# Kernel tuning notes

Hardware: AMD Instinct MI355X
Metric: run time of the kernel (lower is better)

Reference implementation:

```python
import jax, jax.numpy as jnp
import numpy as np

BN_EPS = 1e-5


def setup_inputs() -> dict:
    key = jax.random.key(0)
    ks = jax.random.split(key, 8)
    B, C, N = 2, 64, 8192
    s = 1.0 / np.sqrt(C)
    return {
        "feature": jax.random.normal(ks[0], (B, C, N, 1), dtype=jnp.float32),
        "wa": jax.random.normal(ks[1], (C, C), dtype=jnp.float32) * s,
        "ba": jnp.zeros((C,), jnp.float32),
        "wb": jax.random.normal(ks[2], (C, C), dtype=jnp.float32) * s,
        "bb": jnp.zeros((C,), jnp.float32),
        "wm": jax.random.normal(ks[3], (C, C), dtype=jnp.float32) * s,
        "bm": jnp.zeros((C,), jnp.float32),
        "bn_gamma": jnp.ones((C,), jnp.float32),
        "bn_beta": jnp.zeros((C,), jnp.float32),
        "bn_mean": jax.random.normal(ks[4], (C,), dtype=jnp.float32) * 0.1,
        "bn_var": jnp.ones((C,), jnp.float32) + jax.random.uniform(ks[5], (C,), dtype=jnp.float32),
        "alpha": jnp.array(0.5, jnp.float32),
    }


def _pam(feature, wa, ba, wb, bb, wm, bm, g, bt, mean, var, alpha):
    # feature: [B, C, N, 1]
    x = feature[..., 0]  # [B, C, N]
    a = jnp.einsum('oc,bcn->bon', wa, x) + ba[None, :, None]  # fc_a, 1x1 conv
    b = jnp.einsum('oc,bcn->bon', wb, x) + bb[None, :, None]  # fc_b
    # att = a^T b : [B, N, N], softmax over last dim (dim=2)
    att = jax.nn.softmax(jnp.einsum('bcn,bcm->bnm', a, b), axis=2)
    # mlp branch: 1x1 conv + inference BatchNorm
    m = jnp.einsum('oc,bcn->bon', wm, x) + bm[None, :, None]
    m = (m - mean[None, :, None]) * jax.lax.rsqrt(var + BN_EPS)[None, :, None]
    m = m * g[None, :, None] + bt[None, :, None]
    # (att @ m^T)^T : out[b,c,n] = sum_m att[b,n,m] * m[b,c,m]
    out = jnp.einsum('bnm,bcm->bcn', att, m)
    return feature + alpha * out[..., None]


def reference(feature, wa, ba, wb, bb, wm, bm, bn_gamma, bn_beta, bn_mean, bn_var, alpha):
    # GFA calls self.pam twice (fam is unused in its forward): f1 + f2 == 2 * pam(feature)
    p = _pam(feature, wa, ba, wb, bb, wm, bm, bn_gamma, bn_beta, bn_mean, bn_var, alpha)
    return p + p
```

## Files before the change

### kernel.cpp

```cpp
#include <hip/hip_runtime.h>
#include <hip/hip_bf16.h>
#include <math.h>

#define CDIM 64
#define BATCH 2
#define KSPLIT 8
#define TK 64
#define M_FIX 44.0f
#define LOG2E 1.44269504f

typedef __bf16 bf16x8 __attribute__((ext_vector_type(8)));
typedef __bf16 bf16x4 __attribute__((ext_vector_type(4)));
typedef float f32x4 __attribute__((ext_vector_type(4)));
typedef float f32x16 __attribute__((ext_vector_type(16)));

__global__ __launch_bounds__(256) void gfa_stage1(
    const float* __restrict__ feature,
    const float* __restrict__ wa, const float* __restrict__ ba,
    const float* __restrict__ wb, const float* __restrict__ bb,
    const float* __restrict__ wm, const float* __restrict__ bm,
    const float* __restrict__ gma, const float* __restrict__ bta,
    const float* __restrict__ mean, const float* __restrict__ var,
    __bf16* __restrict__ Q, __bf16* __restrict__ K, __bf16* __restrict__ V,
    int N)
{
    const int tid  = threadIdx.x;
    const int w    = tid >> 6;
    const int lane = tid & 63;
    const int l15  = lane & 15;
    const int quad = lane >> 4;
    const int n0    = blockIdx.x * 64;
    const int which = blockIdx.y;
    const int b     = blockIdx.z;

    __shared__ __align__(16) char s1lds[35328];
    float*  Xs  = (float*)s1lds;
    __bf16* Whi = (__bf16*)(s1lds + 16896);
    __bf16* Wlo = (__bf16*)(s1lds + 26112);
    __bf16* Ts  = (__bf16*)s1lds;

    const float* wsel = (which == 0) ? wa : (which == 1) ? wb : wm;
    const float* bsel = (which == 0) ? ba : (which == 1) ? bb : bm;
    const float wscale = (which == 1) ? LOG2E : 1.0f;

    const float* fb = feature + (size_t)b * CDIM * N;
#pragma unroll
    for (int p = 0; p < 4; p++) {
        int idx = p * 256 + tid;
        int c = idx >> 4, n4 = (idx & 15) << 2;
        float4 v = *(const float4*)&fb[(size_t)c * N + n0 + n4];
        *(float2*)&Xs[c * 66 + n4]     = make_float2(v.x, v.y);
        *(float2*)&Xs[c * 66 + n4 + 2] = make_float2(v.z, v.w);
    }
#pragma unroll
    for (int p = 0; p < 4; p++) {
        int idx = p * 256 + tid;
        int o = idx >> 4, c4 = (idx & 15) << 2;
        float4 v = *(const float4*)&wsel[o * 64 + c4];
        bf16x4 hi, lo;
        float vv[4] = {v.x * wscale, v.y * wscale, v.z * wscale, v.w * wscale};
#pragma unroll
        for (int r = 0; r < 4; r++) {
            hi[r] = (__bf16)vv[r];
            lo[r] = (__bf16)(vv[r] - (float)hi[r]);
        }
        *(bf16x4*)&Whi[o * 72 + c4] = hi;
        *(bf16x4*)&Wlo[o * 72 + c4] = lo;
    }
    __syncthreads();

    const int nb = w * 16;
    bf16x8 xh[2], xl[2];
#pragma unroll
    for (int kc = 0; kc < 2; kc++) {
#pragma unroll
        for (int j = 0; j < 8; j++) {
            float xv = Xs[(kc * 32 + quad * 8 + j) * 66 + nb + l15];
            __bf16 h = (__bf16)xv;
            xh[kc][j] = h;
            xl[kc][j] = (__bf16)(xv - (float)h);
        }
    }

    f32x4 acc[4];
#pragma unroll
    for (int ot = 0; ot < 4; ot++) acc[ot] = (f32x4){0.f, 0.f, 0.f, 0.f};

#pragma unroll
    for (int ot = 0; ot < 4; ot++) {
#pragma unroll
        for (int kc = 0; kc < 2; kc++) {
            bf16x8 wh = *(const bf16x8*)&Whi[(ot * 16 + l15) * 72 + kc * 32 + quad * 8];
            bf16x8 wl = *(const bf16x8*)&Wlo[(ot * 16 + l15) * 72 + kc * 32 + quad * 8];
            acc[ot] = __builtin_amdgcn_mfma_f32_16x16x32_bf16(wh, xh[kc], acc[ot], 0, 0, 0);
            acc[ot] = __builtin_amdgcn_mfma_f32_16x16x32_bf16(wl, xh[kc], acc[ot], 0, 0, 0);
            acc[ot] = __builtin_amdgcn_mfma_f32_16x16x32_bf16(wh, xl[kc], acc[ot], 0, 0, 0);
        }
    }

    __syncthreads();
    if (which < 2) {
        __bf16* O = (which == 0 ? Q : K) + (size_t)b * N * CDIM;
#pragma unroll
        for (int ot = 0; ot < 4; ot++) {
            int o0 = ot * 16 + quad * 4;
            float4 b4 = *(const float4*)&bsel[o0];
            float bv[4] = {b4.x * wscale, b4.y * wscale, b4.z * wscale, b4.w * wscale};
            bf16x4 pk;
#pragma unroll
            for (int r = 0; r < 4; r++) pk[r] = (__bf16)(acc[ot][r] + bv[r]);
            *(bf16x4*)&Ts[(nb + l15) * 68 + o0] = pk;
        }
        __syncthreads();
#pragma unroll
        for (int p = 0; p < 2; p++) {
            int idx = p * 256 + tid;
            int row = idx >> 3, c8 = (idx & 7) * 8;
            *(int4*)&O[(size_t)(n0 + row) * CDIM + c8] = *(int4*)&Ts[row * 68 + c8];
        }
    } else {
        __bf16* Vb = V + (size_t)b * CDIM * N;
#pragma unroll
        for (int ot = 0; ot < 4; ot++) {
            int o0 = ot * 16 + quad * 4;
            float4 b4 = *(const float4*)&bsel[o0];
            float4 m4 = *(const float4*)&mean[o0];
            float4 v4 = *(const float4*)&var[o0];
            float4 g4 = *(const float4*)&gma[o0];
            float4 t4 = *(const float4*)&bta[o0];
            float bv[4] = {b4.x, b4.y, b4.z, b4.w};
            float mv[4] = {m4.x, m4.y, m4.z, m4.w};
            float vv[4] = {v4.x, v4.y, v4.z, v4.w};
            float gv[4] = {g4.x, g4.y, g4.z, g4.w};
            float tv[4] = {t4.x, t4.y, t4.z, t4.w};
#pragma unroll
            for (int r = 0; r < 4; r++) {
                float s = gv[r] * rsqrtf(vv[r] + 1e-5f);
                float val = (acc[ot][r] + bv[r] - mv[r]) * s + tv[r];
                Ts[(o0 + r) * 68 + nb + l15] = (__bf16)val;
            }
        }
        __syncthreads();
#pragma unroll
        for (int p = 0; p < 2; p++) {
            int idx = p * 256 + tid;
            int row = idx >> 3, n8 = (idx & 7) * 8;
            *(int4*)&Vb[(size_t)row * N + n0 + n8] = *(int4*)&Ts[row * 68 + n8];
        }
    }
}

__global__ __launch_bounds__(256, 2) void gfa_stage2(
    const __bf16* __restrict__ Q, const __bf16* __restrict__ K,
    const __bf16* __restrict__ V,
    __bf16* __restrict__ Upart, float* __restrict__ stats, int N)
{
    const int tid  = threadIdx.x;
    const int w    = tid >> 6;
    const int lane = tid & 63;
    const int l31  = lane & 31;
    const int half = lane >> 5;
    const int qt_  = blockIdx.x;
    const int sp   = blockIdx.y;
    const int b    = blockIdx.z;
    const int qb   = qt_ * 256 + w * 64;
    const int QT   = N >> 6;

    __shared__ __align__(16) char lds[55296];
    char* Kt = lds;
    char* Vt = lds + 9216;
    char* Pw = lds + 18432 + w * 9216;

    const __bf16* Qg = Q + (size_t)b * N * CDIM;
    const __bf16* Kg = K + (size_t)b * N * CDIM;
    const __bf16* Vg = V + (size_t)b * CDIM * N;
    const int kvb = sp * (N / KSPLIT);
    const int r8 = tid >> 3, c16 = (tid & 7) * 16;

    bf16x8 qf[2][4];
#pragma unroll
    for (int qt = 0; qt < 2; qt++)
#pragma unroll
        for (int kc = 0; kc < 4; kc++)
            qf[qt][kc] = *(const bf16x8*)((const char*)Qg
                + (size_t)(qb + qt * 32 + l31) * 128 + kc * 32 + half * 16);

    f32x16 acc[2][2];
#pragma unroll
    for (int qt = 0; qt < 2; qt++)
#pragma unroll
        for (int ct = 0; ct < 2; ct++)
#pragma unroll
            for (int r = 0; r < 16; r++) acc[qt][ct][r] = 0.f;
    float l_run[2] = {0.f, 0.f};

    const int NIT = N / KSPLIT / TK;
    for (int it = 0; it < NIT; it++) {
        const int kv0 = kvb + it * TK;
        __syncthreads();
#pragma unroll
        for (int p = 0; p < 2; p++) {
            int r = p * 32 + r8;
            *(int4*)(Kt + r * 144 + c16) =
                *(const int4*)((const char*)Kg + (size_t)(kv0 + r) * 128 + c16);
        }
#pragma unroll
        for (int p = 0; p < 2; p++) {
            int r = p * 32 + r8;
            *(int4*)(Vt + r * 144 + c16) =
                *(const int4*)((const char*)Vg + ((size_t)r * N + kv0) * 2 + c16);
        }
        __syncthreads();

#pragma unroll
        for (int kvt = 0; kvt < 2; kvt++) {
            bf16x8 kf[4];
#pragma unroll
            for (int kc = 0; kc < 4; kc++)
                kf[kc] = *(const bf16x8*)(Kt + (kvt * 32 + l31) * 144 + kc * 32 + half * 16);
#pragma unroll
            for (int qt = 0; qt < 2; qt++) {
                f32x16 s16;
#pragma unroll
                for (int r = 0; r < 16; r++) s16[r] = 0.f;
#pragma unroll
                for (int kc = 0; kc < 4; kc++)
                    s16 = __builtin_amdgcn_mfma_f32_32x32x16_bf16(kf[kc], qf[qt][kc], s16, 0, 0, 0);
                float s = 0.f;
#pragma unroll
                for (int rg = 0; rg < 4; rg++) {
                    bf16x4 pb;
#pragma unroll
                    for (int r = 0; r < 4; r++) {
                        float p = __builtin_amdgcn_exp2f(s16[rg * 4 + r] - M_FIX);
                        s += p;
                        pb[r] = (__bf16)p;
                    }
                    *(bf16x4*)(Pw + (qt * 32 + l31) * 144
                               + (kvt * 32 + rg * 8 + half * 4) * 2) = pb;
                }
                l_run[qt] += s;
            }
        }

#pragma unroll
        for (int ks = 0; ks < 4; ks++) {
            bf16x8 vf[2], pf[2];
#pragma unroll
            for (int ct = 0; ct < 2; ct++)
                vf[ct] = *(const bf16x8*)(Vt + (ct * 32 + l31) * 144 + ks * 32 + half * 16);
#pragma unroll
            for (int qt = 0; qt < 2; qt++)
                pf[qt] = *(const bf16x8*)(Pw + (qt * 32 + l31) * 144 + ks * 32 + half * 16);
#pragma unroll
            for (int qt = 0; qt < 2; qt++)
#pragma unroll
                for (int ct = 0; ct < 2; ct++)
                    acc[qt][ct] = __builtin_amdgcn_mfma_f32_32x32x16_bf16(vf[ct], pf[qt], acc[qt][ct], 0, 0, 0);
        }
    }

    const int qt64 = qt_ * 4 + w;
    __bf16* Ub = Upart + ((size_t)(b * KSPLIT + sp) * QT + qt64) * 4096;
    float*  Sb = stats + ((size_t)(b * KSPLIT + sp) * QT + qt64) * 64;
#pragma unroll
    for (int qt = 0; qt < 2; qt++) {
        float s = l_run[qt] + __shfl_xor(l_run[qt], 32);
        int qq = qt * 32 + l31;
#pragma unroll
        for (int ct = 0; ct < 2; ct++)
#pragma unroll
            for (int r = 0; r < 16; r++) {
                int c = ct * 32 + (r & 3) + 8 * (r >> 2) + 4 * half;
                Ub[c * 64 + qq] = (__bf16)acc[qt][ct][r];
            }
        if (half == 0) Sb[qq] = s;
    }
}

__global__ __launch_bounds__(256) void gfa_reduce(
    const float* __restrict__ feature, const float* __restrict__ alpha_p,
    const __bf16* __restrict__ Upart, const float* __restrict__ stats,
    float* __restrict__ out, int N)
{
    const int qt = blockIdx.x;
    const int cq = blockIdx.y;
    const int b  = blockIdx.z;
    const int q  = threadIdx.x & 63;
    const int c0 = cq * 16 + (threadIdx.x >> 6) * 4;
    const int QT = N >> 6;

    float L = 0.f;
#pragma unroll
    for (int s = 0; s < KSPLIT; s++)
        L += stats[((size_t)(b * KSPLIT + s) * QT + qt) * 64 + q];

    float u[4] = {0.f, 0.f, 0.f, 0.f};
#pragma unroll
    for (int s = 0; s < KSPLIT; s++) {
        const __bf16* Ub = Upart + ((size_t)(b * KSPLIT + s) * QT + qt) * 4096;
#pragma unroll
        for (int i = 0; i < 4; i++)
            u[i] += (float)Ub[(c0 + i) * 64 + q];
    }

    float scale = 2.f * alpha_p[0] / L;
    const int n = qt * 64 + q;
#pragma unroll
    for (int i = 0; i < 4; i++) {
        size_t gi = ((size_t)b * CDIM + c0 + i) * N + n;
        out[gi] = 2.f * feature[gi] + scale * u[i];
    }
}

extern "C" void kernel_launch(void* const* d_in, const int* in_sizes, int n_in,
                              void* d_out, int out_size, void* d_ws, size_t ws_size,
                              hipStream_t stream) {
    const float* feature = (const float*)d_in[0];
    const float* wa   = (const float*)d_in[1];
    const float* ba   = (const float*)d_in[2];
    const float* wb   = (const float*)d_in[3];
    const float* bb   = (const float*)d_in[4];
    const float* wm   = (const float*)d_in[5];
    const float* bm   = (const float*)d_in[6];
    const float* gma  = (const float*)d_in[7];
    const float* bta  = (const float*)d_in[8];
    const float* mean = (const float*)d_in[9];
    const float* var  = (const float*)d_in[10];
    const float* alpha = (const float*)d_in[11];
    const int N = in_sizes[0] / (BATCH * CDIM);

    __bf16* Q = (__bf16*)d_ws;
    __bf16* K = Q + (size_t)BATCH * N * CDIM;
    __bf16* V = K + (size_t)BATCH * N * CDIM;
    __bf16* Upart = V + (size_t)BATCH * N * CDIM;
    float* stats = (float*)(Upart + (size_t)BATCH * KSPLIT * (N / 64) * 4096);

    dim3 g1(N / 64, 3, BATCH);
    gfa_stage1<<<g1, 256, 0, stream>>>(feature, wa, ba, wb, bb, wm, bm,
                                       gma, bta, mean, var, Q, K, V, N);
    dim3 g2(N / 256, KSPLIT, BATCH);
    gfa_stage2<<<g2, 256, 0, stream>>>(Q, K, V, Upart, stats, N);
    dim3 g3(N / 64, 4, BATCH);
    gfa_reduce<<<g3, 256, 0, stream>>>(feature, alpha, Upart, stats, (float*)d_out, N);
}
```

Measured before the change: 129.7 us.

## Double-buffer K/V tiles with register prefetch and interleave PV per subtile

The attention stage now loads the next K/V tile from global memory into registers while the current tile is being computed. It alternates between two LDS buffers, so each iteration needs one barrier instead of two. The per-warp P scratch is cut to a 32-column tile, and the P·V MFMAs run right after each 32-key subtile's softmax instead of after the whole tile. The aim is to hide global load latency and reduce barrier stalls, at the cost of extra registers for the prefetch and split 8-byte LDS reads for P.

```diff
diff --git a/kernel.cpp b/kernel.cpp
--- a/kernel.cpp
+++ b/kernel.cpp
@@ -167,9 +167,7 @@
     const int QT   = N >> 6;
 
     __shared__ __align__(16) char lds[55296];
-    char* Kt = lds;
-    char* Vt = lds + 9216;
-    char* Pw = lds + 18432 + w * 9216;
+    char* Pw = lds + 36864 + w * 4608;
 
     const __bf16* Qg = Q + (size_t)b * N * CDIM;
     const __bf16* Kg = K + (size_t)b * N * CDIM;
@@ -194,23 +192,32 @@
             for (int r = 0; r < 16; r++) acc[qt][ct][r] = 0.f;
     float l_run[2] = {0.f, 0.f};
 
+    int4 kr[2], vr[2];
+#pragma unroll
+    for (int p = 0; p < 2; p++) {
+        kr[p] = *(const int4*)((const char*)Kg + (size_t)(kvb + p * 32 + r8) * 128 + c16);
+        vr[p] = *(const int4*)((const char*)Vg + ((size_t)(p * 32 + r8) * N + kvb) * 2 + c16);
+    }
+
     const int NIT = N / KSPLIT / TK;
     for (int it = 0; it < NIT; it++) {
-        const int kv0 = kvb + it * TK;
+        char* Kt = lds + (it & 1) * 18432;
+        char* Vt = Kt + 9216;
+#pragma unroll
+        for (int p = 0; p < 2; p++) {
+            *(int4*)(Kt + (p * 32 + r8) * 144 + c16) = kr[p];
+            *(int4*)(Vt + (p * 32 + r8) * 144 + c16) = vr[p];
+        }
         __syncthreads();
-#pragma unroll
-        for (int p = 0; p < 2; p++) {
-            int r = p * 32 + r8;
-            *(int4*)(Kt + r * 144 + c16) =
-                *(const int4*)((const char*)Kg + (size_t)(kv0 + r) * 128 + c16);
-        }
-#pragma unroll
-        for (int p = 0; p < 2; p++) {
-            int r = p * 32 + r8;
-            *(int4*)(Vt + r * 144 + c16) =
-                *(const int4*)((const char*)Vg + ((size_t)r * N + kv0) * 2 + c16);
-        }
-        __syncthreads();
+
+        if (it + 1 < NIT) {
+            const int kv1 = kvb + (it + 1) * TK;
+#pragma unroll
+            for (int p = 0; p < 2; p++) {
+                kr[p] = *(const int4*)((const char*)Kg + (size_t)(kv1 + p * 32 + r8) * 128 + c16);
+                vr[p] = *(const int4*)((const char*)Vg + ((size_t)(p * 32 + r8) * N + kv1) * 2 + c16);
+            }
+        }
 
 #pragma unroll
         for (int kvt = 0; kvt < 2; kvt++) {
@@ -236,27 +243,31 @@
                         s += p;
                         pb[r] = (__bf16)p;
                     }
-                    *(bf16x4*)(Pw + (qt * 32 + l31) * 144
-                               + (kvt * 32 + rg * 8 + half * 4) * 2) = pb;
+                    *(bf16x4*)(Pw + (qt * 32 + l31) * 72 + rg * 16 + half * 8) = pb;
                 }
                 l_run[qt] += s;
             }
-        }
-
-#pragma unroll
-        for (int ks = 0; ks < 4; ks++) {
-            bf16x8 vf[2], pf[2];
-#pragma unroll
-            for (int ct = 0; ct < 2; ct++)
-                vf[ct] = *(const bf16x8*)(Vt + (ct * 32 + l31) * 144 + ks * 32 + half * 16);
-#pragma unroll
-            for (int qt = 0; qt < 2; qt++)
-                pf[qt] = *(const bf16x8*)(Pw + (qt * 32 + l31) * 144 + ks * 32 + half * 16);
-#pragma unroll
-            for (int qt = 0; qt < 2; qt++)
+#pragma unroll
+            for (int ks = 0; ks < 2; ks++) {
+                bf16x8 vfv[2], pfv[2];
 #pragma unroll
                 for (int ct = 0; ct < 2; ct++)
-                    acc[qt][ct] = __builtin_amdgcn_mfma_f32_32x32x16_bf16(vf[ct], pf[qt], acc[qt][ct], 0, 0, 0);
+                    vfv[ct] = *(const bf16x8*)(Vt + (ct * 32 + l31) * 144
+                                               + kvt * 64 + ks * 32 + half * 16);
+#pragma unroll
+                for (int qt = 0; qt < 2; qt++) {
+                    const char* pr = Pw + (qt * 32 + l31) * 72 + ks * 32 + half * 16;
+                    bf16x4 plo = *(const bf16x4*)(pr);
+                    bf16x4 phi = *(const bf16x4*)(pr + 8);
+#pragma unroll
+                    for (int j = 0; j < 4; j++) { pfv[qt][j] = plo[j]; pfv[qt][j + 4] = phi[j]; }
+                }
+#pragma unroll
+                for (int qt = 0; qt < 2; qt++)
+#pragma unroll
+                    for (int ct = 0; ct < 2; ct++)
+                        acc[qt][ct] = __builtin_amdgcn_mfma_f32_32x32x16_bf16(vfv[ct], pfv[qt], acc[qt][ct], 0, 0, 0);
+            }
         }
     }
 
```

New measurement: 157.4 us. +21.4%, slower.

## Fuse split-K reduction into attention kernel via atomic last-block counter

Applied to the files above, without the earlier changes.

Removes the separate reduce kernel. Each attention block now bumps a per-query-tile atomic counter, and the last of the KSPLIT blocks sums the partials and writes the output. It also shrinks the LDS row pitch from 144 to 136 bytes and raises launch bounds to 3 blocks per CU to allow higher occupancy. The cost is a memset launch, threadfences, and a serialized reduce tail in the last block, and the new pitch may change LDS bank conflicts.

```diff
diff --git a/kernel.cpp b/kernel.cpp
--- a/kernel.cpp
+++ b/kernel.cpp
@@ -150,10 +150,13 @@
     }
 }
 
-__global__ __launch_bounds__(256, 2) void gfa_stage2(
+__global__ __launch_bounds__(256, 3) void gfa_stage2(
     const __bf16* __restrict__ Q, const __bf16* __restrict__ K,
     const __bf16* __restrict__ V,
-    __bf16* __restrict__ Upart, float* __restrict__ stats, int N)
+    __bf16* __restrict__ Upart, float* __restrict__ stats,
+    int* __restrict__ counters,
+    const float* __restrict__ feature, const float* __restrict__ alpha_p,
+    float* __restrict__ out, int N)
 {
     const int tid  = threadIdx.x;
     const int w    = tid >> 6;
@@ -165,11 +168,13 @@
     const int b    = blockIdx.z;
     const int qb   = qt_ * 256 + w * 64;
     const int QT   = N >> 6;
-
-    __shared__ __align__(16) char lds[55296];
+    const int QT256 = N >> 8;
+
+    __shared__ __align__(16) char lds[52224];
+    __shared__ int is_last;
     char* Kt = lds;
-    char* Vt = lds + 9216;
-    char* Pw = lds + 18432 + w * 9216;
+    char* Vt = lds + 8704;
+    char* Pw = lds + 17408 + w * 8704;
 
     const __bf16* Qg = Q + (size_t)b * N * CDIM;
     const __bf16* Kg = K + (size_t)b * N * CDIM;
@@ -201,13 +206,13 @@
 #pragma unroll
         for (int p = 0; p < 2; p++) {
             int r = p * 32 + r8;
-            *(int4*)(Kt + r * 144 + c16) =
+            *(int4*)(Kt + r * 136 + c16) =
                 *(const int4*)((const char*)Kg + (size_t)(kv0 + r) * 128 + c16);
         }
 #pragma unroll
         for (int p = 0; p < 2; p++) {
             int r = p * 32 + r8;
-            *(int4*)(Vt + r * 144 + c16) =
+            *(int4*)(Vt + r * 136 + c16) =
                 *(const int4*)((const char*)Vg + ((size_t)r * N + kv0) * 2 + c16);
         }
         __syncthreads();
@@ -217,7 +222,7 @@
             bf16x8 kf[4];
 #pragma unroll
             for (int kc = 0; kc < 4; kc++)
-                kf[kc] = *(const bf16x8*)(Kt + (kvt * 32 + l31) * 144 + kc * 32 + half * 16);
+                kf[kc] = *(const bf16x8*)(Kt + (kvt * 32 + l31) * 136 + kc * 32 + half * 16);
 #pragma unroll
             for (int qt = 0; qt < 2; qt++) {
                 f32x16 s16;
@@ -236,7 +241,7 @@
                         s += p;
                         pb[r] = (__bf16)p;
                     }
-                    *(bf16x4*)(Pw + (qt * 32 + l31) * 144
+                    *(bf16x4*)(Pw + (qt * 32 + l31) * 136
                                + (kvt * 32 + rg * 8 + half * 4) * 2) = pb;
                 }
                 l_run[qt] += s;
@@ -248,10 +253,10 @@
             bf16x8 vf[2], pf[2];
 #pragma unroll
             for (int ct = 0; ct < 2; ct++)
-                vf[ct] = *(const bf16x8*)(Vt + (ct * 32 + l31) * 144 + ks * 32 + half * 16);
+                vf[ct] = *(const bf16x8*)(Vt + (ct * 32 + l31) * 136 + ks * 32 + half * 16);
 #pragma unroll
             for (int qt = 0; qt < 2; qt++)
-                pf[qt] = *(const bf16x8*)(Pw + (qt * 32 + l31) * 144 + ks * 32 + half * 16);
+                pf[qt] = *(const bf16x8*)(Pw + (qt * 32 + l31) * 136 + ks * 32 + half * 16);
 #pragma unroll
             for (int qt = 0; qt < 2; qt++)
 #pragma unroll
@@ -276,40 +281,38 @@
             }
         if (half == 0) Sb[qq] = s;
     }
-}
-
-__global__ __launch_bounds__(256) void gfa_reduce(
-    const float* __restrict__ feature, const float* __restrict__ alpha_p,
-    const __bf16* __restrict__ Upart, const float* __restrict__ stats,
-    float* __restrict__ out, int N)
-{
-    const int qt = blockIdx.x;
-    const int cq = blockIdx.y;
-    const int b  = blockIdx.z;
-    const int q  = threadIdx.x & 63;
-    const int c0 = cq * 16 + (threadIdx.x >> 6) * 4;
-    const int QT = N >> 6;
-
-    float L = 0.f;
-#pragma unroll
-    for (int s = 0; s < KSPLIT; s++)
-        L += stats[((size_t)(b * KSPLIT + s) * QT + qt) * 64 + q];
-
-    float u[4] = {0.f, 0.f, 0.f, 0.f};
-#pragma unroll
-    for (int s = 0; s < KSPLIT; s++) {
-        const __bf16* Ub = Upart + ((size_t)(b * KSPLIT + s) * QT + qt) * 4096;
-#pragma unroll
-        for (int i = 0; i < 4; i++)
-            u[i] += (float)Ub[(c0 + i) * 64 + q];
-    }
-
-    float scale = 2.f * alpha_p[0] / L;
-    const int n = qt * 64 + q;
-#pragma unroll
-    for (int i = 0; i < 4; i++) {
-        size_t gi = ((size_t)b * CDIM + c0 + i) * N + n;
-        out[gi] = 2.f * feature[gi] + scale * u[i];
+
+    __threadfence();
+    if (tid == 0) {
+        int old = atomicAdd(&counters[b * QT256 + qt_], 1);
+        is_last = (old == KSPLIT - 1);
+    }
+    __syncthreads();
+    if (!is_last) return;
+    __threadfence();
+
+    const int qq = tid & 63;
+    const int cg = tid >> 6;
+    const float a2 = 2.f * alpha_p[0];
+#pragma unroll
+    for (int t4 = 0; t4 < 4; t4++) {
+        const int qt64r = qt_ * 4 + t4;
+        float L = 0.f;
+#pragma unroll
+        for (int s = 0; s < KSPLIT; s++)
+            L += stats[((size_t)(b * KSPLIT + s) * QT + qt64r) * 64 + qq];
+        const float scale = a2 / L;
+        const int n = qt64r * 64 + qq;
+#pragma unroll
+        for (int i = 0; i < 16; i++) {
+            const int c = cg * 16 + i;
+            float u = 0.f;
+#pragma unroll
+            for (int s = 0; s < KSPLIT; s++)
+                u += (float)Upart[((size_t)(b * KSPLIT + s) * QT + qt64r) * 4096 + c * 64 + qq];
+            const size_t gi = ((size_t)b * CDIM + c) * N + n;
+            out[gi] = 2.f * feature[gi] + scale * u;
+        }
     }
 }
 
@@ -335,12 +338,14 @@
     __bf16* V = K + (size_t)BATCH * N * CDIM;
     __bf16* Upart = V + (size_t)BATCH * N * CDIM;
     float* stats = (float*)(Upart + (size_t)BATCH * KSPLIT * (N / 64) * 4096);
+    int* counters = (int*)(stats + (size_t)BATCH * KSPLIT * (N / 64) * 64);
+
+    hipMemsetAsync(counters, 0, BATCH * (N / 256) * sizeof(int), stream);
 
     dim3 g1(N / 64, 3, BATCH);
     gfa_stage1<<<g1, 256, 0, stream>>>(feature, wa, ba, wb, bb, wm, bm,
                                        gma, bta, mean, var, Q, K, V, N);
     dim3 g2(N / 256, KSPLIT, BATCH);
-    gfa_stage2<<<g2, 256, 0, stream>>>(Q, K, V, Upart, stats, N);
-    dim3 g3(N / 64, 4, BATCH);
-    gfa_reduce<<<g3, 256, 0, stream>>>(feature, alpha, Upart, stats, (float*)d_out, N);
+    gfa_stage2<<<g2, 256, 0, stream>>>(Q, K, V, Upart, stats, counters,
+                                       feature, alpha, (float*)d_out, N);
 }
```

Result: slower. 290.7 us (+124.2%).
